# Kernel tuning notes

Measured on AMD Instinct MI355X. Metric: run time of the kernel, lower is better.

The kernel has to match this reference:

```python
import jax, jax.numpy as jnp
import numpy as np

N, CIN, COUT, K = 16384, 3, 3, 20

def prelu(x, a):
    return jnp.maximum(x, 0) + a * jnp.minimum(x, 0)

def knn_ind(x, k):
    # pairwise squared distances; topk of -d includes self (d=0), matching torch
    xx = jnp.sum(x * x, axis=1, keepdims=True)          # [n,1]
    d = xx + xx.T - 2.0 * (x @ x.T)                      # [n,n]
    return jax.lax.top_k(-d, k)[1]                       # [n,k] int32

def graph_features(x, k):
    ind = knn_ind(x, k)                                  # [n,k]
    xi = x[ind]                                          # [n,k,C] gather
    x_ = jnp.broadcast_to(x[:, None, :], xi.shape)       # [n,k,C]
    return jnp.concatenate([xi - x_, x_], axis=-1)       # [n,k,2C]

def edge_conv(x, k, layers):
    f = graph_features(x, k)                             # [n,k,2C]
    for (W, a) in layers:
        f = prelu(f @ W, a)
    return jnp.max(f, axis=-2)                           # [n,Cout] max over k neighbors

def setup_inputs() -> dict:
    key = jax.random.key(0)
    ks = jax.random.split(key, 16)
    def w(kk, i, o):
        return jax.random.normal(kk, (i, o), jnp.float32) * (1.0 / np.sqrt(i))
    p = jnp.float32(0.25)
    return {
        "x": jax.random.normal(ks[0], (N, CIN), jnp.float32),
        "hidden": jax.random.normal(ks[1], (1,), jnp.float32),
        "W1a": w(ks[2], 2 * CIN, 64), "p1a": p,
        "W1b": w(ks[3], 64, 64),      "p1b": p,
        "W2a": w(ks[4], 128, 64),     "p2a": p,
        "W2b": w(ks[5], 64, 64),      "p2b": p,
        "W3":  w(ks[6], 128, 64),     "p3": p,
        "W4":  w(ks[7], 192, 1024),   "p4": p,
        "W5":  w(ks[8], 1024 + 192, 256), "p5": p,
        "W6":  w(ks[9], 256, 256),    "p6": p,
        "W7":  w(ks[10], 256, 128),   "p7": p,
        "W8":  w(ks[11], 128, COUT),  "p8": p,
    }

def reference(x, hidden, W1a, p1a, W1b, p1b, W2a, p2a, W2b, p2b, W3, p3,
              W4, p4, W5, p5, W6, p6, W7, p7, W8, p8):
    n = x.shape[0]
    x1 = edge_conv(x, K, [(W1a, p1a), (W1b, p1b)])       # [n,64]
    x2 = edge_conv(x1, K, [(W2a, p2a), (W2b, p2b)])      # [n,64]
    x3 = edge_conv(x2, K, [(W3, p3)])                    # [n,64]
    x4 = jnp.concatenate([x1, x2, x3], axis=-1)          # [n,192]
    x5 = prelu(x4 @ W4, p4)                              # [n,1024]
    x5 = jnp.broadcast_to(jnp.max(x5, axis=0, keepdims=True), (n, 1024))
    h = jnp.concatenate([x1, x2, x3, x5], axis=-1)       # [n,1216]
    h = prelu(h @ W5, p5)                                # dropout = identity (eval)
    h = prelu(h @ W6, p6)
    h = prelu(h @ W7, p7)
    h = prelu(h @ W8, p8)                                # [n,COUT]
    return (h, hidden)
```

## Files before the change

kernel.cpp:

```cpp
#include <hip/hip_runtime.h>
#include <hip/hip_bf16.h>
#include <float.h>

#define NPTS 16384
#define KK 20
#define COUT 3
#define SURV_CAP 256

typedef float f4 __attribute__((ext_vector_type(4)));
typedef float f32x4 __attribute__((ext_vector_type(4)));
typedef short bh8 __attribute__((ext_vector_type(8)));

__device__ __forceinline__ void ins20(float (&td)[KK], float &kmax, float nd) {
  float cd = nd;
#pragma unroll
  for (int j = 0; j < KK; ++j) {
    float t0 = td[j];
    bool lt = cd < t0;
    td[j] = lt ? cd : t0;
    cd = lt ? t0 : cd;
  }
  kmax = td[KK - 1];
}

__device__ __forceinline__ void ins4(float (&td)[4], float &kmax, float nd) {
  float cd = nd;
#pragma unroll
  for (int j = 0; j < 4; ++j) {
    float t0 = td[j];
    bool lt = cd < t0;
    td[j] = lt ? cd : t0;
    cd = lt ? t0 : cd;
  }
  kmax = td[3];
}

__device__ __forceinline__ void ins20p(float (&td)[KK], int (&ti)[KK],
                                       float &kmax, float nd, int ni) {
  float cd = nd; int ci = ni;
#pragma unroll
  for (int j = 0; j < KK; ++j) {
    float t0 = td[j]; int t1 = ti[j];
    bool lt = cd < t0;
    td[j] = lt ? cd : t0;  ti[j] = lt ? ci : t1;
    cd = lt ? t0 : cd;     ci = lt ? t1 : ci;
  }
  kmax = td[KK - 1];
}

template<int C>
__global__ void norms_kernel(const float* __restrict__ X, int ldx, float* __restrict__ vn) {
  int i = blockIdx.x * 256 + threadIdx.x;
  if (i >= NPTS) return;
  const float* row = X + (size_t)i * ldx;
  float s = 0.f;
#pragma unroll
  for (int c = 0; c < C; ++c) s = fmaf(row[c], row[c], s);
  vn[i] = s;
}

__global__ __launch_bounds__(256)
void mean64_kernel(const float* __restrict__ X, int ldx, float* __restrict__ mean) {
  __shared__ float p[256];
  const int d = blockIdx.x, t = threadIdx.x;
  float s = 0.f;
  for (int r = t; r < NPTS; r += 256) s += X[(size_t)r * ldx + d];
  p[t] = s;
  __syncthreads();
  for (int o = 128; o > 0; o >>= 1) { if (t < o) p[t] += p[t + o]; __syncthreads(); }
  if (t == 0) mean[d] = p[0] * (1.0f / NPTS);
}

__global__ __launch_bounds__(256)
void xc_kernel(const float* __restrict__ X, int ldx, const float* __restrict__ mean,
               float* __restrict__ Xc, short* __restrict__ Xbf,
               float* __restrict__ vn, float* __restrict__ sn) {
  __shared__ float msh[64];
  const int t = threadIdx.x;
  if (t < 64) msh[t] = mean[t];
  __syncthreads();
  const int row = blockIdx.x * 32 + (t >> 3), sub = t & 7;
  f4 a = *(const f4*)&X[(size_t)row * ldx + sub * 8];
  f4 b = *(const f4*)&X[(size_t)row * ldx + sub * 8 + 4];
#pragma unroll
  for (int e = 0; e < 4; ++e) { a[e] -= msh[sub * 8 + e]; b[e] -= msh[sub * 8 + 4 + e]; }
  *(f4*)&Xc[(size_t)row * 64 + sub * 8] = a;
  *(f4*)&Xc[(size_t)row * 64 + sub * 8 + 4] = b;
  bh8 o;
#pragma unroll
  for (int e = 0; e < 4; ++e) {
    __hip_bfloat16 ha = __float2bfloat16(a[e]);
    __hip_bfloat16 hb = __float2bfloat16(b[e]);
    o[e] = *reinterpret_cast<short*>(&ha);
    o[4 + e] = *reinterpret_cast<short*>(&hb);
  }
  *(bh8*)&Xbf[(size_t)row * 64 + sub * 8] = o;
  float s = a[0]*a[0] + a[1]*a[1] + a[2]*a[2] + a[3]*a[3]
          + b[0]*b[0] + b[1]*b[1] + b[2]*b[2] + b[3]*b[3];
  s += __shfl_xor(s, 1);
  s += __shfl_xor(s, 2);
  s += __shfl_xor(s, 4);
  if (sub == 0) { vn[row] = s; sn[row] = sqrtf(s); }
}

template<int C>
__global__ __launch_bounds__(256, 2)
void sampleTv4_kernel(const float* __restrict__ X, const float* __restrict__ vn,
                      float* __restrict__ plist) {
  __shared__ __align__(16) float Qs[C * 64];
  __shared__ __align__(16) float Cs[C * 132];
  __shared__ float cn[128];
  const int t = threadIdx.x;
  const int qb = blockIdx.x * 64;
  const int tb = blockIdx.y ? 11 : 0;
  const int nt = blockIdx.y ? 10 : 11;

  if constexpr (C == 64) {
#pragma unroll
    for (int u = 0; u < 4; ++u) {
      int idx = u * 256 + t;
      int q = idx & 63, dg = idx >> 6;
      f4 v = *(const f4*)&X[(size_t)(qb + q) * C + dg * 4];
#pragma unroll
      for (int e = 0; e < 4; ++e) Qs[(dg * 4 + e) * 64 + q] = v[e];
    }
  } else {
    for (int idx = t; idx < C * 64; idx += 256) {
      int q = idx & 63, d = idx >> 6;
      Qs[d * 64 + q] = X[(size_t)(qb + q) * C + d];
    }
  }

  const int tq = t & 15, tc = t >> 4;
  const int q0 = tq * 4, c0 = tc * 8;

  float l4[4][4]; float km[4];
#pragma unroll
  for (int i = 0; i < 4; ++i) {
    km[i] = FLT_MAX;
#pragma unroll
    for (int k = 0; k < 4; ++k) l4[i][k] = FLT_MAX;
  }

  for (int tt = 0; tt < nt; ++tt) {
    const int base = (tb + tt) * 128;
    __syncthreads();
    if constexpr (C == 64) {
#pragma unroll
      for (int u = 0; u < 8; ++u) {
        int idx = u * 256 + t;
        int r = idx & 127, dg = idx >> 7;
        f4 v = *(const f4*)&X[(size_t)((base + r) * 6) * C + dg * 4];
#pragma unroll
        for (int e = 0; e < 4; ++e) Cs[(dg * 4 + e) * 132 + r] = v[e];
      }
    } else {
      for (int idx = t; idx < C * 128; idx += 256) {
        int r = idx & 127, d = idx >> 7;
        Cs[d * 132 + r] = X[(size_t)((base + r) * 6) * C + d];
      }
    }
    if (t < 128) cn[t] = vn[(base + t) * 6];
    __syncthreads();

    float acc[4][8];
#pragma unroll
    for (int i = 0; i < 4; ++i)
#pragma unroll
      for (int j = 0; j < 8; ++j) acc[i][j] = 0.f;

#pragma unroll 4
    for (int d = 0; d < C; ++d) {
      f4 qa = *(const f4*)&Qs[d * 64 + q0];
      f4 ca = *(const f4*)&Cs[d * 132 + c0];
      f4 cb = *(const f4*)&Cs[d * 132 + c0 + 4];
      float cr[8] = {ca[0], ca[1], ca[2], ca[3], cb[0], cb[1], cb[2], cb[3]};
#pragma unroll
      for (int i = 0; i < 4; ++i)
#pragma unroll
        for (int j = 0; j < 8; ++j)
          acc[i][j] = fmaf(qa[i], cr[j], acc[i][j]);
    }

#pragma unroll
    for (int j = 0; j < 8; ++j) {
      float cv = cn[c0 + j];
#pragma unroll
      for (int i = 0; i < 4; ++i) {
        float sv = fmaf(-2.f, acc[i][j], cv);
        if (sv < km[i]) ins4(l4[i], km[i], sv);
      }
    }
  }

#pragma unroll
  for (int i = 0; i < 4; ++i) {
    size_t off = (((size_t)blockIdx.y * NPTS + (qb + q0 + i)) * 16 + tc) * 4;
    f4 v = {l4[i][0], l4[i][1], l4[i][2], l4[i][3]};
    *(f4*)&plist[off] = v;
  }
}

__global__ __launch_bounds__(256)
void mergeT_kernel(const float* __restrict__ plist, float* __restrict__ T,
                   unsigned* __restrict__ cnt, unsigned* __restrict__ redoCnt) {
  const int q = blockIdx.x * 256 + threadIdx.x;
  float td[KK];
#pragma unroll
  for (int j = 0; j < KK; ++j) td[j] = FLT_MAX;
  float km = FLT_MAX;
  for (int s = 0; s < 2; ++s) {
    const float* p = &plist[((size_t)s * NPTS + q) * 64];
    for (int z = 0; z < 64; ++z) {
      float v = p[z];
      if (v < km) ins20(td, km, v);
    }
  }
  T[q] = td[KK - 1] + 1e-4f * (fabsf(td[KK - 1]) + 1.0f);
  cnt[q] = 0u;
  if (q == 0) *redoCnt = 0u;
}

template<int C>
__global__ __launch_bounds__(256, 2)
void knn_filter_kernel(const float* __restrict__ X, int ldx, const float* __restrict__ vn,
                       const float* __restrict__ T,
                       float* __restrict__ survd, int* __restrict__ survi,
                       unsigned* __restrict__ cnt) {
  constexpr int QT = 128, CT = 128, CSTR = CT + 4;
  constexpr int KC = (C < 32) ? C : 32;
  constexpr int NCH = (C + KC - 1) / KC;
  constexpr int CAPB = 40;
  __shared__ __align__(16) float Qs[KC * QT];
  __shared__ __align__(16) float Cs[KC * CSTR];
  __shared__ float cnorm[CT];
  __shared__ float Tsl[QT];
  __shared__ unsigned scnt[QT];
  __shared__ float sbD[QT * CAPB];
  __shared__ int   sbI[QT * CAPB];

  const int t = threadIdx.x;
  const int qb = blockIdx.x * QT;
  const int cbase = blockIdx.y * (NPTS / 8);

  if (t < QT) { Tsl[t] = T[qb + t]; scnt[t] = 0u; }

  const int tq = t & 15, tc = t >> 4;
  const int q0 = tq * 8, c0 = tc * 8;

  for (int ct = 0; ct < (NPTS / 8) / CT; ++ct) {
    const int cb = cbase + ct * CT;

    float acc[8][8];
#pragma unroll
    for (int i = 0; i < 8; ++i)
#pragma unroll
      for (int j = 0; j < 8; ++j) acc[i][j] = 0.f;

    for (int kc = 0; kc < NCH; ++kc) {
      __syncthreads();
      for (int idx = t; idx < KC * QT; idx += 256) {
        int q = idx / KC, c = idx - q * KC;
        Qs[c * QT + q] = X[(size_t)(qb + q) * ldx + kc * KC + c];
      }
      for (int idx = t; idx < KC * CT; idx += 256) {
        int j = idx / KC, c = idx - j * KC;
        Cs[c * CSTR + j] = X[(size_t)(cb + j) * ldx + kc * KC + c];
      }
      if (kc == 0 && t < CT) cnorm[t] = vn[cb + t];
      __syncthreads();

#pragma unroll 2
      for (int d = 0; d < KC; ++d) {
        f4 qa = *(const f4*)&Qs[d * QT + q0];
        f4 qbv = *(const f4*)&Qs[d * QT + q0 + 4];
        f4 ca = *(const f4*)&Cs[d * CSTR + c0];
        f4 cbv = *(const f4*)&Cs[d * CSTR + c0 + 4];
        float qr[8] = {qa[0], qa[1], qa[2], qa[3], qbv[0], qbv[1], qbv[2], qbv[3]};
        float cr[8] = {ca[0], ca[1], ca[2], ca[3], cbv[0], cbv[1], cbv[2], cbv[3]};
#pragma unroll
        for (int i = 0; i < 8; ++i)
#pragma unroll
          for (int j = 0; j < 8; ++j)
            acc[i][j] = fmaf(qr[i], cr[j], acc[i][j]);
      }
    }

#pragma unroll
    for (int j = 0; j < 8; ++j) {
      float cv = cnorm[c0 + j];
#pragma unroll
      for (int i = 0; i < 8; ++i)
        acc[i][j] = fmaf(-2.f, acc[i][j], cv);
    }
#pragma unroll
    for (int i = 0; i < 8; ++i) {
      const float tcut = Tsl[q0 + i];
      const int q = qb + q0 + i;
#pragma unroll
      for (int j = 0; j < 8; ++j) {
        if (acc[i][j] <= tcut) {
          unsigned p = atomicAdd(&scnt[q0 + i], 1u);
          if (p < CAPB) {
            sbD[(q0 + i) * CAPB + p] = acc[i][j];
            sbI[(q0 + i) * CAPB + p] = cb + c0 + j;
          } else {
            unsigned gp = atomicAdd(&cnt[q], 1u);
            if (gp < SURV_CAP) {
              survd[(size_t)q * SURV_CAP + gp] = acc[i][j];
              survi[(size_t)q * SURV_CAP + gp] = cb + c0 + j;
            }
          }
        }
      }
    }
  }

  __syncthreads();
  if (t < QT) {
    unsigned n = scnt[t]; if (n > CAPB) n = CAPB;
    if (n) {
      unsigned base = atomicAdd(&cnt[qb + t], n);
      for (unsigned i = 0; i < n; ++i) {
        unsigned p = base + i;
        if (p < SURV_CAP) {
          survd[(size_t)(qb + t) * SURV_CAP + p] = sbD[t * CAPB + i];
          survi[(size_t)(qb + t) * SURV_CAP + p] = sbI[t * CAPB + i];
        }
      }
    }
  }
}

__global__ __launch_bounds__(256, 2)
void knn_filter64_mfma(const short* __restrict__ Xbf, const float* __restrict__ vn,
                       const float* __restrict__ sn, const float* __restrict__ T,
                       int* __restrict__ survi, unsigned* __restrict__ cnt) {
  __shared__ __align__(16) short Qs[128 * 64];
  __shared__ __align__(16) short Cs[128 * 64];
  __shared__ float vnc[128], snq[128], snc[128], Tq[128];
  __shared__ unsigned scnt[128];
  __shared__ int sbI[128 * 8];

  const int t = threadIdx.x;
  const int qb = blockIdx.x * 128, cb = blockIdx.y * 128;

#pragma unroll
  for (int p = 0; p < 4; ++p) {
    int idx = p * 256 + t;
    int row = idx >> 3, sl = idx & 7;
    int slq = sl ^ (row & 7);
    *(bh8*)&Qs[row * 64 + slq * 8] = *(const bh8*)&Xbf[(size_t)(qb + row) * 64 + sl * 8];
    *(bh8*)&Cs[row * 64 + slq * 8] = *(const bh8*)&Xbf[(size_t)(cb + row) * 64 + sl * 8];
  }
  if (t < 128) { Tq[t] = T[qb + t]; snq[t] = sn[qb + t]; scnt[t] = 0u; }
  else { vnc[t - 128] = vn[cb + t - 128]; snc[t - 128] = sn[cb + t - 128]; }
  __syncthreads();

  const int w = t >> 6, l = t & 63;
  const int qsub = (w >> 1) * 64, csub = (w & 1) * 64;
  const int lr = l & 15, lh = l >> 4;

  f32x4 acc[4][4];
#pragma unroll
  for (int i = 0; i < 4; ++i)
#pragma unroll
    for (int j = 0; j < 4; ++j) acc[i][j] = f32x4{0.f, 0.f, 0.f, 0.f};

#pragma unroll
  for (int kk = 0; kk < 2; ++kk) {
    const int sl = kk * 4 + lh;
    bh8 af[4], bf[4];
#pragma unroll
    for (int i = 0; i < 4; ++i) {
      int qr = qsub + i * 16 + lr;
      af[i] = *(const bh8*)&Qs[qr * 64 + (sl ^ (qr & 7)) * 8];
      int cr = csub + i * 16 + lr;
      bf[i] = *(const bh8*)&Cs[cr * 64 + (sl ^ (cr & 7)) * 8];
    }
#pragma unroll
    for (int i = 0; i < 4; ++i)
#pragma unroll
      for (int j = 0; j < 4; ++j)
        acc[i][j] = __builtin_amdgcn_mfma_f32_16x16x32_bf16(af[i], bf[j], acc[i][j], 0, 0, 0);
  }

#pragma unroll
  for (int i = 0; i < 4; ++i) {
#pragma unroll
    for (int r = 0; r < 4; ++r) {
      const int ql = qsub + i * 16 + lh * 4 + r;
      const float tcut = Tq[ql];
      const float sq = snq[ql];
      const int q = qb + ql;
#pragma unroll
      for (int j = 0; j < 4; ++j) {
        const int cl = csub + j * 16 + lr;
        float s = fmaf(-2.f, acc[i][j][r], vnc[cl]);
        float margin = 0.0082f * sq * snc[cl] + 1e-6f;
        if (s <= tcut + margin) {
          unsigned p = atomicAdd(&scnt[ql], 1u);
          if (p < 8u) sbI[ql * 8 + p] = cb + cl;
          else {
            unsigned gp = atomicAdd(&cnt[q], 1u);
            if (gp < SURV_CAP) survi[(size_t)q * SURV_CAP + gp] = cb + cl;
          }
        }
      }
    }
  }

  __syncthreads();
  if (t < 128) {
    unsigned n = scnt[t]; if (n > 8u) n = 8u;
    if (n) {
      unsigned base = atomicAdd(&cnt[qb + t], n);
      for (unsigned i = 0; i < n; ++i) {
        unsigned p = base + i;
        if (p < SURV_CAP) survi[(size_t)(qb + t) * SURV_CAP + p] = sbI[t * 8 + i];
      }
    }
  }
}

template<int C>
__global__ __launch_bounds__(256, 2)
void exact_kernel(const float* __restrict__ X, int ldx, const float* __restrict__ vn,
                  const unsigned* __restrict__ cnt, const int* __restrict__ survi,
                  float* __restrict__ survd) {
  __shared__ float qsh[C];
  const int q = blockIdx.x;
  const int t = threadIdx.x;
  if (t < C) qsh[t] = X[(size_t)q * ldx + t];
  __syncthreads();
  unsigned n = cnt[q];
  if (n > SURV_CAP) n = SURV_CAP;
  if (t < n) {
    const int c = survi[(size_t)q * SURV_CAP + t];
    const float* crow = X + (size_t)c * ldx;
    float d0 = 0.f, d1 = 0.f, d2 = 0.f, d3 = 0.f;
#pragma unroll
    for (int s = 0; s < C / 4; ++s) {
      f4 cv = *(const f4*)&crow[s * 4];
      d0 = fmaf(cv[0], qsh[s * 4 + 0], d0);
      d1 = fmaf(cv[1], qsh[s * 4 + 1], d1);
      d2 = fmaf(cv[2], qsh[s * 4 + 2], d2);
      d3 = fmaf(cv[3], qsh[s * 4 + 3], d3);
    }
    survd[(size_t)q * SURV_CAP + t] = fmaf(-2.f, (d0 + d1) + (d2 + d3), vn[c]);
  }
}

__global__ __launch_bounds__(256, 2)
void select_kernel(const float* __restrict__ survd, const int* __restrict__ survi,
                   const unsigned* __restrict__ cnt, int* __restrict__ ind,
                   unsigned* __restrict__ redoCnt, int* __restrict__ redoList) {
  const int q = blockIdx.x * 256 + threadIdx.x;
  const unsigned n = cnt[q];
  if (n > SURV_CAP) {
    unsigned p = atomicAdd(redoCnt, 1u);
    redoList[p] = q;
    return;
  }
  float td[KK]; int ti[KK];
#pragma unroll
  for (int j = 0; j < KK; ++j) { td[j] = FLT_MAX; ti[j] = 0; }
  float kmax = FLT_MAX;
  for (unsigned i = 0; i < n; ++i) {
    float d = survd[(size_t)q * SURV_CAP + i];
    if (d < kmax) ins20p(td, ti, kmax, d, survi[(size_t)q * SURV_CAP + i]);
  }
#pragma unroll
  for (int j = 0; j < KK; ++j) ind[q * KK + j] = ti[j];
}

template<int C>
__global__ __launch_bounds__(256, 2)
void knn_redo_kernel(const float* __restrict__ X, int ldx, const float* __restrict__ vn,
                     const int* __restrict__ redoList, const unsigned* __restrict__ redoCnt,
                     int* __restrict__ ind) {
  __shared__ float lds_d[256 * KK];
  __shared__ int   lds_i[256 * KK];
  const int t = threadIdx.x;
  const unsigned n = *redoCnt;
  for (unsigned e = blockIdx.x; e < n; e += gridDim.x) {
    const int q = redoList[e];
    float qreg[C];
#pragma unroll
    for (int d = 0; d < C; ++d) qreg[d] = X[(size_t)q * ldx + d];
    float td[KK]; int ti[KK];
#pragma unroll
    for (int j = 0; j < KK; ++j) { td[j] = FLT_MAX; ti[j] = 0; }
    float kmax = FLT_MAX;
    for (int c = t; c < NPTS; c += 256) {
      const float* crow = X + (size_t)c * ldx;
      float d0 = 0.f;
      if constexpr (C >= 4) {
        float d1 = 0.f, d2 = 0.f, d3 = 0.f;
#pragma unroll
        for (int s = 0; s < C / 4; ++s) {
          f4 cv = *(const f4*)&crow[s * 4];
          d0 = fmaf(cv[0], qreg[s * 4 + 0], d0);
          d1 = fmaf(cv[1], qreg[s * 4 + 1], d1);
          d2 = fmaf(cv[2], qreg[s * 4 + 2], d2);
          d3 = fmaf(cv[3], qreg[s * 4 + 3], d3);
        }
        d0 = (d0 + d1) + (d2 + d3);
      } else {
#pragma unroll
        for (int d = 0; d < C; ++d) d0 = fmaf(crow[d], qreg[d], d0);
      }
      float sv = fmaf(-2.f, d0, vn[c]);
      if (sv < kmax) ins20p(td, ti, kmax, sv, c);
    }
#pragma unroll
    for (int j = 0; j < KK; ++j) { lds_d[t * KK + j] = td[j]; lds_i[t * KK + j] = ti[j]; }
    __syncthreads();
#pragma unroll
    for (int G = 1; G <= 64; G *= 4) {
      const int nth = 64 / ((G == 64) ? 64 : (G == 16) ? 16 : (G == 4) ? 4 : 1);
      if (t < nth) {
        float md[KK]; int mi[KK];
#pragma unroll
        for (int j = 0; j < KK; ++j) { md[j] = FLT_MAX; mi[j] = 0; }
        float km = FLT_MAX;
        for (int s = 0; s < 4; ++s) {
          int base = ((t * 4 + s) * G) * KK;
          for (int j = 0; j < KK; ++j) {
            float v = lds_d[base + j];
            if (v < km) ins20p(md, mi, km, v, lds_i[base + j]);
            else break;
          }
        }
        int obase = (t * 4 * G) * KK;
#pragma unroll
        for (int j = 0; j < KK; ++j) { lds_d[obase + j] = md[j]; lds_i[obase + j] = mi[j]; }
      }
      __syncthreads();
    }
    if (t == 0) {
#pragma unroll
      for (int j = 0; j < KK; ++j) ind[q * KK + j] = lds_i[j];
    }
    __syncthreads();
  }
}

template<int CIN>
__global__ __launch_bounds__(256, 2)
void ub_kernel(const float* __restrict__ X, int ldx, const float* __restrict__ W1,
               float* __restrict__ UB) {
  __shared__ __align__(16) float Ws[2 * CIN * 64];
  __shared__ __align__(16) float Xs[32][(CIN == 3) ? 4 : CIN];
  const int t = threadIdx.x;
  for (int idx = t; idx < 2 * CIN * 64; idx += 256) Ws[idx] = W1[idx];
  const int pb = blockIdx.x * 32;
  if constexpr (CIN == 64) {
    int r = t >> 3, g = t & 7;
    f4 a = *(const f4*)&X[(size_t)(pb + r) * ldx + g * 8];
    f4 b = *(const f4*)&X[(size_t)(pb + r) * ldx + g * 8 + 4];
    *(f4*)&Xs[r][g * 8] = a;
    *(f4*)&Xs[r][g * 8 + 4] = b;
  } else {
    if (t < 32 * CIN) {
      int r = t / CIN, d = t - r * CIN;
      Xs[r][d] = X[(size_t)(pb + r) * ldx + d];
    }
  }
  __syncthreads();
  const int p = t >> 3, c0 = (t & 7) * 8;
  float u[8], v[8];
#pragma unroll
  for (int e = 0; e < 8; ++e) { u[e] = 0.f; v[e] = 0.f; }
#pragma unroll 4
  for (int k = 0; k < CIN; ++k) {
    float xv = Xs[p][k];
    f4 wt0 = *(const f4*)&Ws[k * 64 + c0];
    f4 wt1 = *(const f4*)&Ws[k * 64 + c0 + 4];
    f4 wb0 = *(const f4*)&Ws[(CIN + k) * 64 + c0];
    f4 wb1 = *(const f4*)&Ws[(CIN + k) * 64 + c0 + 4];
#pragma unroll
    for (int e = 0; e < 4; ++e) {
      u[e]     = fmaf(xv, wt0[e], u[e]);
      u[4 + e] = fmaf(xv, wt1[e], u[4 + e]);
      v[e]     = fmaf(xv, wb0[e], v[e]);
      v[4 + e] = fmaf(xv, wb1[e], v[4 + e]);
    }
  }
  float* o = &UB[(size_t)(pb + p) * 128];
  f4 a0 = {u[0], u[1], u[2], u[3]}, a1 = {u[4], u[5], u[6], u[7]};
  f4 b0 = {v[0] - u[0], v[1] - u[1], v[2] - u[2], v[3] - u[3]};
  f4 b1 = {v[4] - u[4], v[5] - u[5], v[6] - u[6], v[7] - u[7]};
  *(f4*)&o[c0] = a0;       *(f4*)&o[c0 + 4] = a1;
  *(f4*)&o[64 + c0] = b0;  *(f4*)&o[64 + c0 + 4] = b1;
}

__global__ __launch_bounds__(256, 3)
void edgeconv2_kernel(const float* __restrict__ UB, const int* __restrict__ ind,
                      const float* __restrict__ W2, const float* __restrict__ p1p,
                      const float* __restrict__ p2p,
                      float* __restrict__ Y, int ldy) {
  __shared__ __align__(16) float W2s[64 * 64];
  __shared__ __align__(16) float h1[4][64 * 32];
  __shared__ float Bs[4][64];
  __shared__ int nbs[4][KK];
  const int t = threadIdx.x;
  const int w = t >> 6, l = t & 63;
  const float a1 = *p1p, a2 = *p2p;
  const int i = blockIdx.x * 4 + w;
  for (int idx = t; idx < 64 * 64; idx += 256) W2s[idx] = W2[idx];
  if (l < 16) *(f4*)&Bs[w][l * 4] = *(const f4*)&UB[(size_t)i * 128 + 64 + l * 4];
  if (l < KK) nbs[w][l] = ind[i * KK + l];
  __syncthreads();

  {
    const int kslot = l >> 1, ch0 = (l & 1) * 32;
    if (kslot < KK) {
      const int nb = nbs[w][kslot];
      const float* ur = &UB[(size_t)nb * 128 + ch0];
#pragma unroll
      for (int g = 0; g < 8; ++g) {
        f4 uv = *(const f4*)&ur[g * 4];
#pragma unroll
        for (int e = 0; e < 4; ++e) {
          int c = ch0 + g * 4 + e;
          float hv = uv[e] + Bs[w][c];
          hv = fmaxf(hv, 0.f) + a1 * fminf(hv, 0.f);
          h1[w][c * 32 + kslot] = hv;
        }
      }
    } else {
#pragma unroll
      for (int g = 0; g < 32; ++g) h1[w][(ch0 + g) * 32 + kslot] = 0.f;
    }
  }
  __syncthreads();

  const int kg = l >> 3, cg = l & 7;
  const int k0 = kg * 4, c0 = cg * 8;
  float acc[4][8];
#pragma unroll
  for (int a = 0; a < 4; ++a)
#pragma unroll
    for (int b = 0; b < 8; ++b) acc[a][b] = 0.f;
#pragma unroll 4
  for (int c = 0; c < 64; ++c) {
    f4 hv = *(const f4*)&h1[w][c * 32 + k0];
    f4 w0 = *(const f4*)&W2s[c * 64 + c0];
    f4 w1 = *(const f4*)&W2s[c * 64 + c0 + 4];
    float wr[8] = {w0[0], w0[1], w0[2], w0[3], w1[0], w1[1], w1[2], w1[3]};
#pragma unroll
    for (int a = 0; a < 4; ++a)
#pragma unroll
      for (int b = 0; b < 8; ++b)
        acc[a][b] = fmaf(hv[a], wr[b], acc[a][b]);
  }

  float mx[8];
#pragma unroll
  for (int b = 0; b < 8; ++b) mx[b] = -FLT_MAX;
  if (kg < 5) {
#pragma unroll
    for (int a = 0; a < 4; ++a)
#pragma unroll
      for (int b = 0; b < 8; ++b) {
        float v = fmaxf(acc[a][b], 0.f) + a2 * fminf(acc[a][b], 0.f);
        mx[b] = fmaxf(mx[b], v);
      }
  }
#pragma unroll
  for (int b = 0; b < 8; ++b) {
    mx[b] = fmaxf(mx[b], __shfl_xor(mx[b], 8));
    mx[b] = fmaxf(mx[b], __shfl_xor(mx[b], 16));
    mx[b] = fmaxf(mx[b], __shfl_xor(mx[b], 32));
  }
  if (kg == 0) {
    f4 o0 = {mx[0], mx[1], mx[2], mx[3]}, o1 = {mx[4], mx[5], mx[6], mx[7]};
    float* yp = &Y[(size_t)i * ldy + c0];
    *(f4*)yp = o0;
    *(f4*)(yp + 4) = o1;
  }
}

__global__ __launch_bounds__(256, 4)
void edgeconv1_kernel(const float* __restrict__ UB, const int* __restrict__ ind,
                      const float* __restrict__ p1p, float* __restrict__ Y, int ldy) {
  __shared__ int nbs[4][KK];
  __shared__ float Bs[4][64];
  const int t = threadIdx.x;
  const int w = t >> 6, l = t & 63;
  const float a1 = *p1p;
  const int i = blockIdx.x * 4 + w;
  if (l < KK) nbs[w][l] = ind[i * KK + l];
  if (l < 16) *(f4*)&Bs[w][l * 4] = *(const f4*)&UB[(size_t)i * 128 + 64 + l * 4];
  __syncthreads();
  const float b = Bs[w][l];
  float mx = -FLT_MAX;
#pragma unroll 4
  for (int k = 0; k < KK; ++k) {
    float uv = UB[(size_t)nbs[w][k] * 128 + l];
    float hv = uv + b;
    hv = fmaxf(hv, 0.f) + a1 * fminf(hv, 0.f);
    mx = fmaxf(mx, hv);
  }
  Y[(size_t)i * ldy + l] = mx;
}

__device__ __forceinline__ unsigned fenc(float f) {
  unsigned u = __float_as_uint(f);
  return (u & 0x80000000u) ? ~u : (u | 0x80000000u);
}
__device__ __forceinline__ float fdec(unsigned u) {
  return (u & 0x80000000u) ? __uint_as_float(u & 0x7fffffffu) : __uint_as_float(~u);
}

__global__ void initg_kernel(unsigned* __restrict__ g) {
  g[blockIdx.x * 256 + threadIdx.x] = 0x007FFFFFu;
}

template<int MODE>
__global__ __launch_bounds__(256, 2)
void gemm_kernel(const float* __restrict__ A, int lda,
                 const float* __restrict__ W, int ldw,
                 const float* __restrict__ bias,
                 const float* __restrict__ pptr,
                 float* __restrict__ Cm, int ldc, int Ktot,
                 unsigned* __restrict__ gmax) {
  __shared__ __align__(16) float At[16 * 132];
  __shared__ __align__(16) float Ws[16 * 128];
  const int t = threadIdx.x;
  const int rb = blockIdx.x * 128, cbb = blockIdx.y * 128;
  const int r0 = (t & 15) * 8, c0 = (t >> 4) * 8;
  const float aa = *pptr;

  float acc[8][8];
#pragma unroll
  for (int i = 0; i < 8; ++i)
#pragma unroll
    for (int j = 0; j < 8; ++j) acc[i][j] = 0.f;

  const int sr = t >> 1, skh = (t & 1) * 8;
  const int wk = t >> 4, wc = (t & 15) * 8;

  for (int k0 = 0; k0 < Ktot; k0 += 16) {
    __syncthreads();
    {
      const float* ap = &A[(size_t)(rb + sr) * lda + k0 + skh];
      f4 v0 = *(const f4*)ap;
      f4 v1 = *(const f4*)(ap + 4);
#pragma unroll
      for (int e = 0; e < 4; ++e) {
        At[(skh + e) * 132 + sr] = v0[e];
        At[(skh + 4 + e) * 132 + sr] = v1[e];
      }
      const float* wp = &W[(size_t)(k0 + wk) * ldw + cbb + wc];
      *(f4*)&Ws[wk * 128 + wc] = *(const f4*)wp;
      *(f4*)&Ws[wk * 128 + wc + 4] = *(const f4*)(wp + 4);
    }
    __syncthreads();
#pragma unroll 4
    for (int d = 0; d < 16; ++d) {
      f4 qa = *(const f4*)&At[d * 132 + r0];
      f4 qb = *(const f4*)&At[d * 132 + r0 + 4];
      f4 wa = *(const f4*)&Ws[d * 128 + c0];
      f4 wb = *(const f4*)&Ws[d * 128 + c0 + 4];
      float qr[8] = {qa[0], qa[1], qa[2], qa[3], qb[0], qb[1], qb[2], qb[3]};
      float wr[8] = {wa[0], wa[1], wa[2], wa[3], wb[0], wb[1], wb[2], wb[3]};
#pragma unroll
      for (int i = 0; i < 8; ++i)
#pragma unroll
        for (int j = 0; j < 8; ++j)
          acc[i][j] = fmaf(qr[i], wr[j], acc[i][j]);
    }
  }

  float bv[8];
#pragma unroll
  for (int j = 0; j < 8; ++j) bv[j] = (MODE == 2) ? bias[cbb + c0 + j] : 0.f;
#pragma unroll
  for (int i = 0; i < 8; ++i)
#pragma unroll
    for (int j = 0; j < 8; ++j) {
      float v = acc[i][j] + bv[j];
      acc[i][j] = fmaxf(v, 0.f) + aa * fminf(v, 0.f);
    }

  if (MODE == 1) {
    float cmax[8];
#pragma unroll
    for (int j = 0; j < 8; ++j) {
      cmax[j] = acc[0][j];
#pragma unroll
      for (int i = 1; i < 8; ++i) cmax[j] = fmaxf(cmax[j], acc[i][j]);
    }
    __syncthreads();
#pragma unroll
    for (int j = 0; j < 8; ++j) At[(t & 15) * 132 + c0 + j] = cmax[j];
    __syncthreads();
    if (t < 128) {
      float m = At[t];
      for (int rr = 1; rr < 16; ++rr) m = fmaxf(m, At[rr * 132 + t]);
      atomicMax(&gmax[cbb + t], fenc(m));
    }
  } else {
#pragma unroll
    for (int i = 0; i < 8; ++i) {
      f4 s0 = {acc[i][0], acc[i][1], acc[i][2], acc[i][3]};
      f4 s1 = {acc[i][4], acc[i][5], acc[i][6], acc[i][7]};
      float* cp = &Cm[(size_t)(rb + r0 + i) * ldc + cbb + c0];
      *(f4*)cp = s0;
      *(f4*)(cp + 4) = s1;
    }
  }
}

__global__ void bias5_kernel(const unsigned* __restrict__ gmax, const float* __restrict__ W5,
                             float* __restrict__ bias5) {
  __shared__ float gs[1024];
  __shared__ float pm[4 * 256];
  int t = threadIdx.x;
  gs[t] = fdec(gmax[t]);
  __syncthreads();
  int c = t & 255, p = t >> 8;
  float acc = 0.f;
  for (int j = p * 256; j < p * 256 + 256; ++j)
    acc = fmaf(gs[j], W5[(size_t)(192 + j) * 256 + c], acc);
  pm[p * 256 + c] = acc;
  __syncthreads();
  if (t < 256) bias5[t] = pm[t] + pm[256 + t] + pm[512 + t] + pm[768 + t];
}

__global__ __launch_bounds__(256, 2)
void w8_kernel(const float* __restrict__ A, const float* __restrict__ W8,
               const float* __restrict__ pptr, const float* __restrict__ hidden,
               float* __restrict__ out) {
  __shared__ __align__(16) float As[64 * 132];
  __shared__ float W8s[128 * COUT];
  int t = threadIdx.x;
  int rb = blockIdx.x * 64;
  for (int idx = t; idx < 128 * COUT; idx += 256) W8s[idx] = W8[idx];
  for (int idx = t; idx < 64 * 32; idx += 256) {
    int r = idx >> 5, c4 = idx & 31;
    *(f4*)&As[r * 132 + c4 * 4] = *(const f4*)&A[(size_t)(rb + r) * 128 + c4 * 4];
  }
  const float a = *pptr;
  __syncthreads();
  int r = t >> 2, c = t & 3;
  if (c < COUT) {
    float acc = 0.f;
#pragma unroll 8
    for (int j = 0; j < 128; ++j)
      acc = fmaf(As[r * 132 + j], W8s[j * COUT + c], acc);
    float v = fmaxf(acc, 0.f) + a * fminf(acc, 0.f);
    out[(size_t)(rb + r) * COUT + c] = v;
  }
  if (blockIdx.x == 0 && t == 0) out[(size_t)NPTS * COUT] = hidden[0];
}

extern "C" void kernel_launch(void* const* d_in, const int* in_sizes, int n_in,
                              void* d_out, int out_size, void* d_ws, size_t ws_size,
                              hipStream_t stream) {
  (void)in_sizes; (void)n_in; (void)out_size; (void)ws_size;
  const float* x      = (const float*)d_in[0];
  const float* hidden = (const float*)d_in[1];
  const float* W1a = (const float*)d_in[2];
  const float* p1a = (const float*)d_in[3];
  const float* W1b = (const float*)d_in[4];
  const float* p1b = (const float*)d_in[5];
  const float* W2a = (const float*)d_in[6];
  const float* p2a = (const float*)d_in[7];
  const float* W2b = (const float*)d_in[8];
  const float* p2b = (const float*)d_in[9];
  const float* W3  = (const float*)d_in[10];
  const float* p3  = (const float*)d_in[11];
  const float* W4  = (const float*)d_in[12];
  const float* p4  = (const float*)d_in[13];
  const float* W5  = (const float*)d_in[14];
  const float* p5  = (const float*)d_in[15];
  const float* W6  = (const float*)d_in[16];
  const float* p6  = (const float*)d_in[17];
  const float* W7  = (const float*)d_in[18];
  const float* p7  = (const float*)d_in[19];
  const float* W8  = (const float*)d_in[20];
  const float* p8  = (const float*)d_in[21];
  float* out = (float*)d_out;

  char* ws = (char*)d_ws;
  size_t off = 0;
  auto carve = [&](size_t bytes) -> void* {
    void* p = ws + off;
    off = (off + bytes + 255) & ~(size_t)255;
    return p;
  };
  float*    x4    = (float*)   carve((size_t)NPTS * 192 * 4);
  float*    vn    = (float*)   carve((size_t)NPTS * 4);
  float*    sn    = (float*)   carve((size_t)NPTS * 4);
  int*      ind   = (int*)     carve((size_t)NPTS * KK * 4);
  float*    T     = (float*)   carve((size_t)NPTS * 4);
  unsigned* cnt   = (unsigned*)carve((size_t)NPTS * 4);
  unsigned* redoCnt = (unsigned*)carve(256);
  int*      redoList = (int*)  carve((size_t)NPTS * 4);
  float*    meanb = (float*)   carve(64 * 4);
  float*    Xc    = (float*)   carve((size_t)NPTS * 64 * 4);
  short*    Xbf   = (short*)   carve((size_t)NPTS * 64 * 2);
  float*    plist = (float*)   carve((size_t)2 * NPTS * 64 * 4);
  unsigned* gmax  = (unsigned*)carve(1024 * 4);
  float*    bias5 = (float*)   carve(256 * 4);
  float*    h5    = (float*)   carve((size_t)NPTS * 256 * 4);
  float*    h6    = (float*)   carve((size_t)NPTS * 256 * 4);
  float* survd = h5;
  int*   survi = (int*)h6;
  float* h7 = x4;
  float* UB = plist;

  norms_kernel<3><<<64, 256, 0, stream>>>(x, 3, vn);
  sampleTv4_kernel<3><<<dim3(256, 2), 256, 0, stream>>>(x, vn, plist);
  mergeT_kernel<<<64, 256, 0, stream>>>(plist, T, cnt, redoCnt);
  knn_filter_kernel<3><<<dim3(128, 8), 256, 0, stream>>>(x, 3, vn, T, survd, survi, cnt);
  select_kernel<<<64, 256, 0, stream>>>(survd, survi, cnt, ind, redoCnt, redoList);
  knn_redo_kernel<3><<<1024, 256, 0, stream>>>(x, 3, vn, redoList, redoCnt, ind);
  ub_kernel<3><<<512, 256, 0, stream>>>(x, 3, W1a, UB);
  edgeconv2_kernel<<<4096, 256, 0, stream>>>(UB, ind, W1b, p1a, p1b, x4 + 0, 192);

  mean64_kernel<<<64, 256, 0, stream>>>(x4 + 0, 192, meanb);
  xc_kernel<<<512, 256, 0, stream>>>(x4 + 0, 192, meanb, Xc, Xbf, vn, sn);
  sampleTv4_kernel<64><<<dim3(256, 2), 256, 0, stream>>>(Xc, vn, plist);
  mergeT_kernel<<<64, 256, 0, stream>>>(plist, T, cnt, redoCnt);
  knn_filter64_mfma<<<dim3(128, 128), 256, 0, stream>>>(Xbf, vn, sn, T, survi, cnt);
  exact_kernel<64><<<NPTS, 256, 0, stream>>>(Xc, 64, vn, cnt, survi, survd);
  select_kernel<<<64, 256, 0, stream>>>(survd, survi, cnt, ind, redoCnt, redoList);
  knn_redo_kernel<64><<<1024, 256, 0, stream>>>(Xc, 64, vn, redoList, redoCnt, ind);
  ub_kernel<64><<<512, 256, 0, stream>>>(x4 + 0, 192, W2a, UB);
  edgeconv2_kernel<<<4096, 256, 0, stream>>>(UB, ind, W2b, p2a, p2b, x4 + 64, 192);

  mean64_kernel<<<64, 256, 0, stream>>>(x4 + 64, 192, meanb);
  xc_kernel<<<512, 256, 0, stream>>>(x4 + 64, 192, meanb, Xc, Xbf, vn, sn);
  sampleTv4_kernel<64><<<dim3(256, 2), 256, 0, stream>>>(Xc, vn, plist);
  mergeT_kernel<<<64, 256, 0, stream>>>(plist, T, cnt, redoCnt);
  knn_filter64_mfma<<<dim3(128, 128), 256, 0, stream>>>(Xbf, vn, sn, T, survi, cnt);
  exact_kernel<64><<<NPTS, 256, 0, stream>>>(Xc, 64, vn, cnt, survi, survd);
  select_kernel<<<64, 256, 0, stream>>>(survd, survi, cnt, ind, redoCnt, redoList);
  knn_redo_kernel<64><<<1024, 256, 0, stream>>>(Xc, 64, vn, redoList, redoCnt, ind);
  ub_kernel<64><<<512, 256, 0, stream>>>(x4 + 64, 192, W3, UB);
  edgeconv1_kernel<<<4096, 256, 0, stream>>>(UB, ind, p3, x4 + 128, 192);

  initg_kernel<<<4, 256, 0, stream>>>(gmax);
  gemm_kernel<1><<<dim3(128, 8), 256, 0, stream>>>(x4, 192, W4, 1024, nullptr, p4, nullptr, 0, 192, gmax);

  bias5_kernel<<<1, 1024, 0, stream>>>(gmax, W5, bias5);

  gemm_kernel<2><<<dim3(128, 2), 256, 0, stream>>>(x4, 192, W5, 256, bias5, p5, h5, 256, 192, nullptr);
  gemm_kernel<0><<<dim3(128, 2), 256, 0, stream>>>(h5, 256, W6, 256, nullptr, p6, h6, 256, 256, nullptr);
  gemm_kernel<0><<<dim3(128, 1), 256, 0, stream>>>(h6, 256, W7, 128, nullptr, p7, h7, 128, 256, nullptr);
  w8_kernel<<<256, 256, 0, stream>>>(h7, W8, p8, hidden, out);
}
```

Before: 2.041 ms.

## Split KNN redo queries across 32 blocks each with a two-pass merge

The brute-force redo path for queries that overflow the survivor cap is split so each of the first 256 redo queries is handled by 32 blocks, each scanning a 512-point slice. Per-slice top-20 results go to a workspace, and a second kernel merges them into the final index list. Queries beyond 256 still use the old single-block-per-query loop. This targets poor parallelism when only a few queries need redo, at the cost of launching 8192 mostly-idle blocks and two extra kernel launches per layer.

```diff
diff --git a/kernel.cpp b/kernel.cpp
--- a/kernel.cpp
+++ b/kernel.cpp
@@ -6,6 +6,7 @@
 #define KK 20
 #define COUT 3
 #define SURV_CAP 256
+#define RQSLOTS 256
 
 typedef float f4 __attribute__((ext_vector_type(4)));
 typedef float f32x4 __attribute__((ext_vector_type(4)));
@@ -476,14 +477,115 @@
 
 template<int C>
 __global__ __launch_bounds__(256, 2)
-void knn_redo_kernel(const float* __restrict__ X, int ldx, const float* __restrict__ vn,
-                     const int* __restrict__ redoList, const unsigned* __restrict__ redoCnt,
-                     int* __restrict__ ind) {
+void knn_redo_p1(const float* __restrict__ X, int ldx, const float* __restrict__ vn,
+                 const int* __restrict__ redoList, const unsigned* __restrict__ redoCnt,
+                 float* __restrict__ rpd, int* __restrict__ rpi) {
   __shared__ float lds_d[256 * KK];
   __shared__ int   lds_i[256 * KK];
   const int t = threadIdx.x;
   const unsigned n = *redoCnt;
-  for (unsigned e = blockIdx.x; e < n; e += gridDim.x) {
+  const unsigned e = blockIdx.x >> 5;
+  const int part = blockIdx.x & 31;
+  if (e >= n || e >= (unsigned)RQSLOTS) return;
+  const int q = redoList[e];
+  float qreg[C];
+#pragma unroll
+  for (int d = 0; d < C; ++d) qreg[d] = X[(size_t)q * ldx + d];
+  float td[KK]; int ti[KK];
+#pragma unroll
+  for (int j = 0; j < KK; ++j) { td[j] = FLT_MAX; ti[j] = 0; }
+  float kmax = FLT_MAX;
+  const int cbase = part * 512;
+#pragma unroll
+  for (int u = 0; u < 2; ++u) {
+    const int c = cbase + u * 256 + t;
+    const float* crow = X + (size_t)c * ldx;
+    float d0 = 0.f;
+    if constexpr (C >= 4) {
+      float d1 = 0.f, d2 = 0.f, d3 = 0.f;
+#pragma unroll
+      for (int s = 0; s < C / 4; ++s) {
+        f4 cv = *(const f4*)&crow[s * 4];
+        d0 = fmaf(cv[0], qreg[s * 4 + 0], d0);
+        d1 = fmaf(cv[1], qreg[s * 4 + 1], d1);
+        d2 = fmaf(cv[2], qreg[s * 4 + 2], d2);
+        d3 = fmaf(cv[3], qreg[s * 4 + 3], d3);
+      }
+      d0 = (d0 + d1) + (d2 + d3);
+    } else {
+#pragma unroll
+      for (int d = 0; d < C; ++d) d0 = fmaf(crow[d], qreg[d], d0);
+    }
+    float sv = fmaf(-2.f, d0, vn[c]);
+    if (sv < kmax) ins20p(td, ti, kmax, sv, c);
+  }
+#pragma unroll
+  for (int j = 0; j < KK; ++j) { lds_d[t * KK + j] = td[j]; lds_i[t * KK + j] = ti[j]; }
+  __syncthreads();
+#pragma unroll
+  for (int G = 1; G <= 64; G *= 4) {
+    const int nth = (G == 64) ? 1 : (G == 16) ? 4 : (G == 4) ? 16 : 64;
+    if (t < nth) {
+      float md[KK]; int mi[KK];
+#pragma unroll
+      for (int j = 0; j < KK; ++j) { md[j] = FLT_MAX; mi[j] = 0; }
+      float km = FLT_MAX;
+      for (int s = 0; s < 4; ++s) {
+        int base = ((t * 4 + s) * G) * KK;
+        for (int j = 0; j < KK; ++j) {
+          float v = lds_d[base + j];
+          if (v < km) ins20p(md, mi, km, v, lds_i[base + j]);
+          else break;
+        }
+      }
+      int obase = (t * 4 * G) * KK;
+#pragma unroll
+      for (int j = 0; j < KK; ++j) { lds_d[obase + j] = md[j]; lds_i[obase + j] = mi[j]; }
+    }
+    __syncthreads();
+  }
+  if (t == 0) {
+    size_t off = ((size_t)e * 32 + part) * KK;
+#pragma unroll
+    for (int j = 0; j < KK; ++j) { rpd[off + j] = lds_d[j]; rpi[off + j] = lds_i[j]; }
+  }
+}
+
+__global__ __launch_bounds__(256)
+void knn_redo_p2(const int* __restrict__ redoList, const unsigned* __restrict__ redoCnt,
+                 const float* __restrict__ rpd, const int* __restrict__ rpi,
+                 int* __restrict__ ind) {
+  const unsigned e = blockIdx.x * 256 + threadIdx.x;
+  const unsigned n = *redoCnt;
+  if (e >= n || e >= (unsigned)RQSLOTS) return;
+  const int q = redoList[e];
+  float td[KK]; int ti[KK];
+#pragma unroll
+  for (int j = 0; j < KK; ++j) { td[j] = FLT_MAX; ti[j] = 0; }
+  float kmax = FLT_MAX;
+  for (int p = 0; p < 32; ++p) {
+    const float* dd = &rpd[((size_t)e * 32 + p) * KK];
+    const int* ii = &rpi[((size_t)e * 32 + p) * KK];
+    for (int j = 0; j < KK; ++j) {
+      float v = dd[j];
+      if (v < kmax) ins20p(td, ti, kmax, v, ii[j]);
+      else break;
+    }
+  }
+#pragma unroll
+  for (int j = 0; j < KK; ++j) ind[q * KK + j] = ti[j];
+}
+
+template<int C>
+__global__ __launch_bounds__(256, 2)
+void knn_redo_kernel(const float* __restrict__ X, int ldx, const float* __restrict__ vn,
+                     const int* __restrict__ redoList, const unsigned* __restrict__ redoCnt,
+                     int* __restrict__ ind, unsigned ebase) {
+  __shared__ float lds_d[256 * KK];
+  __shared__ int   lds_i[256 * KK];
+  const int t = threadIdx.x;
+  const unsigned n = *redoCnt;
+  for (unsigned e = ebase + blockIdx.x; e < n; e += gridDim.x) {
     const int q = redoList[e];
     float qreg[C];
 #pragma unroll
@@ -518,7 +620,7 @@
     __syncthreads();
 #pragma unroll
     for (int G = 1; G <= 64; G *= 4) {
-      const int nth = 64 / ((G == 64) ? 64 : (G == 16) ? 16 : (G == 4) ? 4 : 1);
+      const int nth = (G == 64) ? 1 : (G == 16) ? 4 : (G == 4) ? 16 : 64;
       if (t < nth) {
         float md[KK]; int mi[KK];
 #pragma unroll
@@ -900,6 +1002,8 @@
   unsigned* cnt   = (unsigned*)carve((size_t)NPTS * 4);
   unsigned* redoCnt = (unsigned*)carve(256);
   int*      redoList = (int*)  carve((size_t)NPTS * 4);
+  float*    rpd   = (float*)   carve((size_t)RQSLOTS * 32 * KK * 4);
+  int*      rpi   = (int*)     carve((size_t)RQSLOTS * 32 * KK * 4);
   float*    meanb = (float*)   carve(64 * 4);
   float*    Xc    = (float*)   carve((size_t)NPTS * 64 * 4);
   short*    Xbf   = (short*)   carve((size_t)NPTS * 64 * 2);
@@ -918,7 +1022,9 @@
   mergeT_kernel<<<64, 256, 0, stream>>>(plist, T, cnt, redoCnt);
   knn_filter_kernel<3><<<dim3(128, 8), 256, 0, stream>>>(x, 3, vn, T, survd, survi, cnt);
   select_kernel<<<64, 256, 0, stream>>>(survd, survi, cnt, ind, redoCnt, redoList);
-  knn_redo_kernel<3><<<1024, 256, 0, stream>>>(x, 3, vn, redoList, redoCnt, ind);
+  knn_redo_p1<3><<<RQSLOTS * 32, 256, 0, stream>>>(x, 3, vn, redoList, redoCnt, rpd, rpi);
+  knn_redo_p2<<<1, 256, 0, stream>>>(redoList, redoCnt, rpd, rpi, ind);
+  knn_redo_kernel<3><<<256, 256, 0, stream>>>(x, 3, vn, redoList, redoCnt, ind, RQSLOTS);
   ub_kernel<3><<<512, 256, 0, stream>>>(x, 3, W1a, UB);
   edgeconv2_kernel<<<4096, 256, 0, stream>>>(UB, ind, W1b, p1a, p1b, x4 + 0, 192);
 
@@ -929,7 +1035,9 @@
   knn_filter64_mfma<<<dim3(128, 128), 256, 0, stream>>>(Xbf, vn, sn, T, survi, cnt);
   exact_kernel<64><<<NPTS, 256, 0, stream>>>(Xc, 64, vn, cnt, survi, survd);
   select_kernel<<<64, 256, 0, stream>>>(survd, survi, cnt, ind, redoCnt, redoList);
-  knn_redo_kernel<64><<<1024, 256, 0, stream>>>(Xc, 64, vn, redoList, redoCnt, ind);
+  knn_redo_p1<64><<<RQSLOTS * 32, 256, 0, stream>>>(Xc, 64, vn, redoList, redoCnt, rpd, rpi);
+  knn_redo_p2<<<1, 256, 0, stream>>>(redoList, redoCnt, rpd, rpi, ind);
+  knn_redo_kernel<64><<<256, 256, 0, stream>>>(Xc, 64, vn, redoList, redoCnt, ind, RQSLOTS);
   ub_kernel<64><<<512, 256, 0, stream>>>(x4 + 0, 192, W2a, UB);
   edgeconv2_kernel<<<4096, 256, 0, stream>>>(UB, ind, W2b, p2a, p2b, x4 + 64, 192);
 
@@ -940,7 +1048,9 @@
   knn_filter64_mfma<<<dim3(128, 128), 256, 0, stream>>>(Xbf, vn, sn, T, survi, cnt);
   exact_kernel<64><<<NPTS, 256, 0, stream>>>(Xc, 64, vn, cnt, survi, survd);
   select_kernel<<<64, 256, 0, stream>>>(survd, survi, cnt, ind, redoCnt, redoList);
-  knn_redo_kernel<64><<<1024, 256, 0, stream>>>(Xc, 64, vn, redoList, redoCnt, ind);
+  knn_redo_p1<64><<<RQSLOTS * 32, 256, 0, stream>>>(Xc, 64, vn, redoList, redoCnt, rpd, rpi);
+  knn_redo_p2<<<1, 256, 0, stream>>>(redoList, redoCnt, rpd, rpi, ind);
+  knn_redo_kernel<64><<<256, 256, 0, stream>>>(Xc, 64, vn, redoList, redoCnt, ind, RQSLOTS);
   ub_kernel<64><<<512, 256, 0, stream>>>(x4 + 64, 192, W3, UB);
   edgeconv1_kernel<<<4096, 256, 0, stream>>>(UB, ind, p3, x4 + 128, 192);
 
```

Measured after the change: 1.977 ms. -3.1%, faster.
